# Performance work log

Hardware: AMD Instinct MI355X
Metric: run time of the kernel (lower is better)

The kernel has to match this reference:

```python
import jax, jax.numpy as jnp
import numpy as np

N_NODES = 50000
N_EDGES = 800000
IN_CH = 128
OUT_CH = 64
HEADS = 4
NEG_SLOPE = 0.2


def setup_inputs() -> dict:
    key = jax.random.key(0)
    k1, k2, k3, k4, k5, k6 = jax.random.split(key, 6)
    x = jax.random.normal(k1, (N_NODES, IN_CH), dtype=jnp.float32)
    edge_index = jax.random.randint(k2, (2, N_EDGES), 0, N_NODES, dtype=jnp.int64)
    # GATConv params (glorot-ish scale)
    W = jax.random.normal(k3, (HEADS * OUT_CH, IN_CH), dtype=jnp.float32) * (1.0 / np.sqrt(IN_CH))
    att_src = jax.random.normal(k4, (HEADS, OUT_CH), dtype=jnp.float32) * 0.1
    att_dst = jax.random.normal(k5, (HEADS, OUT_CH), dtype=jnp.float32) * 0.1
    bias = jax.random.normal(k6, (HEADS * OUT_CH,), dtype=jnp.float32) * 0.01
    return {"x": x, "edge_index": edge_index, "W": W, "att_src": att_src, "att_dst": att_dst, "bias": bias}


def reference(x, edge_index, W, att_src, att_dst, bias):
    N = x.shape[0]
    H, C = att_src.shape
    # add self loops (PyG GATConv default add_self_loops=True)
    loops = jnp.arange(N, dtype=edge_index.dtype)
    src = jnp.concatenate([edge_index[0], loops])  # [E+N]
    dst = jnp.concatenate([edge_index[1], loops])
    # linear projection -> [N, H, C]
    xl = (x @ W.T).reshape(N, H, C)
    # per-node attention logits [N, H]
    a_src = jnp.einsum('nhc,hc->nh', xl, att_src)
    a_dst = jnp.einsum('nhc,hc->nh', xl, att_dst)
    # edge-wise score, leaky relu
    alpha = jax.nn.leaky_relu(a_src[src] + a_dst[dst], NEG_SLOPE)  # [E+N, H]
    # segment softmax over destination nodes (every node has a self loop -> no empty segments)
    amax = jax.ops.segment_max(alpha, dst, num_segments=N)
    e = jnp.exp(alpha - amax[dst])
    denom = jax.ops.segment_sum(e, dst, num_segments=N)
    coef = e / denom[dst]  # [E+N, H]
    # weighted scatter-aggregate of source features
    out = jax.ops.segment_sum(coef[:, :, None] * xl[src], dst, num_segments=N)  # [N, H, C]
    out = out.reshape(N, H * C) + bias
    # last_layer=False -> ELU activation
    return jax.nn.elu(out)
```

## Files before the change

### kernel.cpp

```cpp
#include <hip/hip_runtime.h>
#include <hip/hip_bf16.h>
#include <math.h>

#define IN_C 128
#define HC   256
#define CH   64
#define NEG  0.2f

typedef __attribute__((ext_vector_type(8))) short short8;
typedef __attribute__((ext_vector_type(4))) float f32x4;
typedef __attribute__((ext_vector_type(2))) float f32x2;

#define TSTRIDE 264

__device__ __forceinline__ float lrelu(float v) { return v > 0.f ? v : NEG * v; }

__device__ __forceinline__ unsigned short f2bf(float f) {
    __hip_bfloat16 h = __float2bfloat16(f);
    return *reinterpret_cast<unsigned short*>(&h);
}
__device__ __forceinline__ unsigned pack2(float lo, float hi) {
    return (unsigned)f2bf(lo) | ((unsigned)f2bf(hi) << 16);
}

__device__ __forceinline__ void fma8pk(f32x2* acc, float wf, const uint4 u) {
    const f32x2 w2 = {wf, wf};
    f32x2 b;
    b.x = __uint_as_float(u.x << 16); b.y = __uint_as_float(u.x & 0xFFFF0000u);
    acc[0] = __builtin_elementwise_fma(w2, b, acc[0]);
    b.x = __uint_as_float(u.y << 16); b.y = __uint_as_float(u.y & 0xFFFF0000u);
    acc[1] = __builtin_elementwise_fma(w2, b, acc[1]);
    b.x = __uint_as_float(u.z << 16); b.y = __uint_as_float(u.z & 0xFFFF0000u);
    acc[2] = __builtin_elementwise_fma(w2, b, acc[2]);
    b.x = __uint_as_float(u.w << 16); b.y = __uint_as_float(u.w & 0xFFFF0000u);
    acc[3] = __builtin_elementwise_fma(w2, b, acc[3]);
}

__global__ void __launch_bounds__(256) k_gemm_deg(
    const float* __restrict__ x, const float* __restrict__ W,
    const float* __restrict__ att_src, const float* __restrict__ att_dst,
    const int* __restrict__ ei, int* __restrict__ deg, int* __restrict__ perm,
    __hip_bfloat16* __restrict__ xlb, float* __restrict__ asrc,
    float* __restrict__ adst, int N, int E, int DB)
{
    __shared__ short Wlds[256 * 128];

    const int t = threadIdx.x;

    if ((int)blockIdx.x < DB) {
        const int stride = DB * 256;
        for (int e = blockIdx.x * 256 + t; e < E; e += stride) {
            const int d = ei[E + e];
            perm[e] = atomicAdd(&deg[d], 1);
        }
        return;
    }

    const int bx   = blockIdx.x - DB;
    const int wv   = t >> 6;
    const int lane = t & 63;
    const int m    = lane & 15;
    const int quad = lane >> 4;
    const int r0   = bx * 64 + wv * 16;

#pragma unroll
    for (int i = 0; i < 16; ++i) {
        const int g   = t + 256 * i;
        const int row = g >> 4;
        const int c   = g & 15;
        const float4 wa = *(const float4*)&W[g * 8];
        const float4 wb = *(const float4*)&W[g * 8 + 4];
        uint4 v;
        v.x = pack2(wa.x, wa.y); v.y = pack2(wa.z, wa.w);
        v.z = pack2(wb.x, wb.y); v.w = pack2(wb.z, wb.w);
        *(uint4*)&Wlds[row * 128 + ((c ^ (row & 15)) * 8)] = v;
    }
    __syncthreads();

    f32x4 acc[16];
#pragma unroll
    for (int tc = 0; tc < 16; ++tc) acc[tc] = (f32x4){0.f, 0.f, 0.f, 0.f};

    const int arow = min(r0 + m, N - 1);
    const float* xrow = &x[(size_t)arow * IN_C];

#pragma unroll
    for (int kc = 0; kc < IN_C; kc += 32) {
        union { short8 v; unsigned u[4]; } a;
        const float4 xa = *(const float4*)&xrow[kc + quad * 8];
        const float4 xb = *(const float4*)&xrow[kc + quad * 8 + 4];
        a.u[0] = pack2(xa.x, xa.y); a.u[1] = pack2(xa.z, xa.w);
        a.u[2] = pack2(xb.x, xb.y); a.u[3] = pack2(xb.z, xb.w);
        const int kchunk = (kc >> 3) + quad;
        const int slotoff = ((kchunk ^ m) * 8);
#pragma unroll
        for (int tc = 0; tc < 16; ++tc) {
            const short8 b = *(const short8*)&Wlds[(tc * 16 + m) * 128 + slotoff];
            acc[tc] = __builtin_amdgcn_mfma_f32_16x16x32_bf16(a.v, b, acc[tc], 0, 0, 0);
        }
    }

    float as_l[16], ad_l[16];
#pragma unroll
    for (int tc = 0; tc < 16; ++tc) {
        as_l[tc] = att_src[tc * 16 + m];
        ad_l[tc] = att_dst[tc * 16 + m];
    }
#pragma unroll
    for (int i = 0; i < 4; ++i) {
        const int grow = r0 + quad * 4 + i;
        const bool ok = grow < N;
        float ps[4] = {0.f, 0.f, 0.f, 0.f};
        float pd[4] = {0.f, 0.f, 0.f, 0.f};
#pragma unroll
        for (int tc = 0; tc < 16; ++tc) {
            const float v = acc[tc][i];
            ps[tc >> 2] = fmaf(v, as_l[tc], ps[tc >> 2]);
            pd[tc >> 2] = fmaf(v, ad_l[tc], pd[tc >> 2]);
        }
#pragma unroll
        for (int msk = 1; msk < 16; msk <<= 1) {
#pragma unroll
            for (int hd = 0; hd < 4; ++hd) {
                ps[hd] += __shfl_xor(ps[hd], msk);
                pd[hd] += __shfl_xor(pd[hd], msk);
            }
        }
        if (m == 0 && ok) {
#pragma unroll
            for (int hd = 0; hd < 4; ++hd) {
                asrc[grow * 4 + hd] = ps[hd];
                adst[grow * 4 + hd] = pd[hd];
            }
        }
    }

    __syncthreads();
#pragma unroll
    for (int i = 0; i < 4; ++i) {
        const int lrow = wv * 16 + quad * 4 + i;
#pragma unroll
        for (int tc = 0; tc < 16; ++tc)
            Wlds[lrow * TSTRIDE + tc * 16 + m] = (short)f2bf(acc[tc][i]);
    }
    __syncthreads();
    const int r0blk = bx * 64;
#pragma unroll
    for (int k2 = 0; k2 < 8; ++k2) {
        const int c   = t + 256 * k2;
        const int row = c >> 5;
        const int off = c & 31;
        if (r0blk + row < N) {
            const uint4 v = *(const uint4*)&Wlds[row * TSTRIDE + off * 8];
            *(uint4*)&xlb[(size_t)(r0blk + row) * HC + off * 8] = v;
        }
    }
}

#define SCAN_TILE 2048
__global__ void __launch_bounds__(256) k_scan(
    const int* __restrict__ deg, int* __restrict__ offs,
    unsigned long long* __restrict__ tstat, int N, int E, int ntiles)
{
    __shared__ int sh[256];
    __shared__ int sh_base;
    const int tile = blockIdx.x;
    const int t = threadIdx.x;
    const int base = tile * SCAN_TILE + t * 8;

    int v[8];
    int tsum = 0;
#pragma unroll
    for (int j = 0; j < 8; ++j) {
        const int idx = base + j;
        v[j] = (idx < N) ? deg[idx] : 0;
        tsum += v[j];
    }
    sh[t] = tsum;
    __syncthreads();
    for (int off = 1; off < 256; off <<= 1) {
        const int u = (t >= off) ? sh[t - off] : 0;
        __syncthreads();
        sh[t] += u;
        __syncthreads();
    }
    const int blockSum = sh[255];
    const int texcl = sh[t] - tsum;

    if (t == 0) {
        int excl = 0;
        if (tile == 0) {
            __hip_atomic_store(&tstat[0], (2ull << 32) | (unsigned)blockSum,
                               __ATOMIC_RELEASE, __HIP_MEMORY_SCOPE_AGENT);
        } else {
            __hip_atomic_store(&tstat[tile], (1ull << 32) | (unsigned)blockSum,
                               __ATOMIC_RELEASE, __HIP_MEMORY_SCOPE_AGENT);
            int pb = tile - 1;
            while (true) {
                const unsigned long long st = __hip_atomic_load(&tstat[pb],
                        __ATOMIC_ACQUIRE, __HIP_MEMORY_SCOPE_AGENT);
                const unsigned state = (unsigned)(st >> 32);
                if (state == 0u) continue;
                excl += (int)(unsigned)(st & 0xFFFFFFFFu);
                if (state == 2u) break;
                --pb;
            }
            __hip_atomic_store(&tstat[tile],
                               (2ull << 32) | (unsigned)(excl + blockSum),
                               __ATOMIC_RELEASE, __HIP_MEMORY_SCOPE_AGENT);
        }
        sh_base = excl;
    }
    __syncthreads();
    int running = sh_base + texcl;
#pragma unroll
    for (int j = 0; j < 8; ++j) {
        const int idx = base + j;
        if (idx < N) offs[idx] = running;
        running += v[j];
    }
    if (tile == ntiles - 1 && t == 255) offs[N] = E;
}

__global__ void k_place(const int* __restrict__ ei, const int* __restrict__ perm,
                        const int* __restrict__ offs, int* __restrict__ csr_src, int E)
{
    int e = blockIdx.x * 256 + threadIdx.x;
    if (e >= E) return;
    int s = ei[e];
    int d = ei[E + e];
    csr_src[offs[d] + perm[e]] = s;
}

__global__ void __launch_bounds__(256, 8) k_agg(
    const __hip_bfloat16* __restrict__ xlb, const float* __restrict__ asrc,
    const float* __restrict__ adst, const int* __restrict__ offs,
    const int* __restrict__ csr_src, const float* __restrict__ bias,
    float* __restrict__ out, int N)
{
    const int t    = threadIdx.x;
    const int wv   = t >> 6;
    const int lane = t & 63;
    const int half = lane >> 5;
    const int li   = lane & 31;
    const int h    = li >> 3;
    const int n    = blockIdx.x * 4 + wv;
    if (n >= N) return;

    const float adn = adst[n * 4 + h];
    const int   p0 = offs[n];
    const int   pe = offs[n + 1];

    f32x2 acc[4];
#pragma unroll
    for (int q = 0; q < 4; ++q) acc[q] = (f32x2){0.f, 0.f};
    float l = 0.f;

    if (half == 0) {
        const float w = __expf(lrelu(asrc[n * 4 + h] + adn));
        const uint4 u = *(const uint4*)&xlb[(unsigned)n * HC + li * 8];
        fma8pk(acc, w, u);
        l = w;
    }

    int p = p0 + half;

    for (; p + 16 <= pe + half; p += 16) {
        int s[8];
#pragma unroll
        for (int j = 0; j < 8; ++j) s[j] = csr_src[p + 2 * j];
        uint4 u[8];
#pragma unroll
        for (int j = 0; j < 8; ++j)
            u[j] = *(const uint4*)&xlb[(unsigned)s[j] * HC + li * 8];
        float w[4];
#pragma unroll
        for (int j = 0; j < 4; ++j)
            w[j] = __expf(lrelu(asrc[s[j] * 4 + h] + adn));
#pragma unroll
        for (int j = 0; j < 4; ++j) { l += w[j]; fma8pk(acc, w[j], u[j]); }
#pragma unroll
        for (int j = 0; j < 4; ++j)
            w[j] = __expf(lrelu(asrc[s[j + 4] * 4 + h] + adn));
#pragma unroll
        for (int j = 0; j < 4; ++j) { l += w[j]; fma8pk(acc, w[j], u[j + 4]); }
    }
    for (; p + 8 <= pe + half; p += 8) {
        int s[4];
#pragma unroll
        for (int j = 0; j < 4; ++j) s[j] = csr_src[p + 2 * j];
        uint4 u[4];
#pragma unroll
        for (int j = 0; j < 4; ++j)
            u[j] = *(const uint4*)&xlb[(unsigned)s[j] * HC + li * 8];
#pragma unroll
        for (int j = 0; j < 4; ++j) {
            const float w = __expf(lrelu(asrc[s[j] * 4 + h] + adn));
            l += w;
            fma8pk(acc, w, u[j]);
        }
    }
    for (; p < pe; p += 2) {
        const int s0 = csr_src[p];
        const uint4 u0 = *(const uint4*)&xlb[(unsigned)s0 * HC + li * 8];
        const float w0 = __expf(lrelu(asrc[s0 * 4 + h] + adn));
        l += w0;
        fma8pk(acc, w0, u0);
    }

    l += __shfl_xor(l, 32);
#pragma unroll
    for (int q = 0; q < 4; ++q) {
        acc[q].x += __shfl_xor(acc[q].x, 32);
        acc[q].y += __shfl_xor(acc[q].y, 32);
    }
    const float inv = 1.0f / l;

    const int cbase = li * 8 + half * 4;
    const float4 bv = *(const float4*)&bias[cbase];
    f32x4 o;
    o.x = acc[half * 2 + 0].x * inv + bv.x;
    o.y = acc[half * 2 + 0].y * inv + bv.y;
    o.z = acc[half * 2 + 1].x * inv + bv.z;
    o.w = acc[half * 2 + 1].y * inv + bv.w;
    o.x = o.x > 0.f ? o.x : expm1f(o.x);
    o.y = o.y > 0.f ? o.y : expm1f(o.y);
    o.z = o.z > 0.f ? o.z : expm1f(o.z);
    o.w = o.w > 0.f ? o.w : expm1f(o.w);
    __builtin_nontemporal_store(o, (f32x4*)&out[(size_t)n * HC + cbase]);
}

extern "C" void kernel_launch(void* const* d_in, const int* in_sizes, int n_in,
                              void* d_out, int out_size, void* d_ws, size_t ws_size,
                              hipStream_t stream) {
    const float* x       = (const float*)d_in[0];
    const int*   ei      = (const int*)d_in[1];
    const float* W       = (const float*)d_in[2];
    const float* att_src = (const float*)d_in[3];
    const float* att_dst = (const float*)d_in[4];
    const float* bias    = (const float*)d_in[5];
    float* out = (float*)d_out;

    const int N = in_sizes[0] / IN_C;
    const int E = in_sizes[1] / 2;

    char* p = (char*)d_ws;
    auto alloc = [&](size_t bytes) -> char* {
        char* q = p;
        p += (bytes + 255) & ~(size_t)255;
        return q;
    };
    __hip_bfloat16* xlb = (__hip_bfloat16*)alloc((size_t)N * HC * 2);
    float* asrc = (float*)alloc((size_t)N * 4 * 4);
    float* adst = (float*)alloc((size_t)N * 4 * 4);
    int*   deg  = (int*)alloc((size_t)N * 4);
    unsigned long long* tstat = (unsigned long long*)alloc(4096);
    int*   offs = (int*)alloc((size_t)(N + 1) * 4);
    int*   perm = (int*)alloc((size_t)E * 4);
    int*   csr  = (int*)alloc((size_t)E * 4);

    const size_t degpad = ((size_t)N * 4 + 255) & ~(size_t)255;
    (void)hipMemsetAsync(deg, 0, degpad + 4096, stream);

    const int GB = (N + 63) / 64;
    const int DB = (E + 2047) / 2048;
    k_gemm_deg<<<DB + GB, 256, 0, stream>>>(x, W, att_src, att_dst,
                                            ei, deg, perm, xlb, asrc, adst, N, E, DB);

    const int ntiles = (N + SCAN_TILE - 1) / SCAN_TILE;
    k_scan<<<ntiles, 256, 0, stream>>>(deg, offs, tstat, N, E, ntiles);

    k_place<<<(E + 255) / 256, 256, 0, stream>>>(ei, perm, offs, csr, E);

    k_agg<<<(N + 3) / 4, 256, 0, stream>>>(xlb, asrc, adst, offs, csr, bias, out, N);
}
```

Before: 226.0 us.

## Pre-convert W to bf16 once and read B fragments from global in GEMM

Splits the fused GEMM+degree kernel into a degree-counting kernel, which also converts W to bf16 once, and a separate GEMM kernel. The GEMM now loads B fragments straight from the cached bf16 W in global memory instead of having every block stage and convert the 64KB W into LDS. That shrinks LDS to the transpose tile and raises occupancy (launch bounds 256,4). It adds a kernel launch and L2 traffic for B loads. k_place also becomes a grid-stride loop over 1024 blocks.

Result: slower. 261.3 us (+15.6%).

```diff
diff --git a/kernel.cpp b/kernel.cpp
--- a/kernel.cpp
+++ b/kernel.cpp
@@ -36,46 +36,44 @@
     acc[3] = __builtin_elementwise_fma(w2, b, acc[3]);
 }
 
-__global__ void __launch_bounds__(256) k_gemm_deg(
-    const float* __restrict__ x, const float* __restrict__ W,
+__global__ void __launch_bounds__(256) k_deg(
+    const float* __restrict__ W, short* __restrict__ Wb,
+    const int* __restrict__ ei, int* __restrict__ deg, int* __restrict__ perm,
+    int E, int WB)
+{
+    const int t = threadIdx.x;
+    if ((int)blockIdx.x < WB) {
+        const int i = (blockIdx.x * 256 + t) * 4;
+        const float4 v = *(const float4*)&W[i];
+        uint2 pk;
+        pk.x = pack2(v.x, v.y);
+        pk.y = pack2(v.z, v.w);
+        *(uint2*)&Wb[i] = pk;
+        return;
+    }
+    const int nb = gridDim.x - WB;
+    const int stride = nb * 256;
+    for (int e = (blockIdx.x - WB) * 256 + t; e < E; e += stride) {
+        const int d = ei[E + e];
+        perm[e] = atomicAdd(&deg[d], 1);
+    }
+}
+
+__global__ void __launch_bounds__(256, 4) k_gemm(
+    const float* __restrict__ x, const short* __restrict__ Wb,
     const float* __restrict__ att_src, const float* __restrict__ att_dst,
-    const int* __restrict__ ei, int* __restrict__ deg, int* __restrict__ perm,
     __hip_bfloat16* __restrict__ xlb, float* __restrict__ asrc,
-    float* __restrict__ adst, int N, int E, int DB)
-{
-    __shared__ short Wlds[256 * 128];
-
-    const int t = threadIdx.x;
-
-    if ((int)blockIdx.x < DB) {
-        const int stride = DB * 256;
-        for (int e = blockIdx.x * 256 + t; e < E; e += stride) {
-            const int d = ei[E + e];
-            perm[e] = atomicAdd(&deg[d], 1);
-        }
-        return;
-    }
-
-    const int bx   = blockIdx.x - DB;
+    float* __restrict__ adst, int N)
+{
+    __shared__ short Tlds[64 * TSTRIDE];
+
+    const int t    = threadIdx.x;
+    const int bx   = blockIdx.x;
     const int wv   = t >> 6;
     const int lane = t & 63;
     const int m    = lane & 15;
     const int quad = lane >> 4;
     const int r0   = bx * 64 + wv * 16;
-
-#pragma unroll
-    for (int i = 0; i < 16; ++i) {
-        const int g   = t + 256 * i;
-        const int row = g >> 4;
-        const int c   = g & 15;
-        const float4 wa = *(const float4*)&W[g * 8];
-        const float4 wb = *(const float4*)&W[g * 8 + 4];
-        uint4 v;
-        v.x = pack2(wa.x, wa.y); v.y = pack2(wa.z, wa.w);
-        v.z = pack2(wb.x, wb.y); v.w = pack2(wb.z, wb.w);
-        *(uint4*)&Wlds[row * 128 + ((c ^ (row & 15)) * 8)] = v;
-    }
-    __syncthreads();
 
     f32x4 acc[16];
 #pragma unroll
@@ -91,12 +89,17 @@
         const float4 xb = *(const float4*)&xrow[kc + quad * 8 + 4];
         a.u[0] = pack2(xa.x, xa.y); a.u[1] = pack2(xa.z, xa.w);
         a.u[2] = pack2(xb.x, xb.y); a.u[3] = pack2(xb.z, xb.w);
-        const int kchunk = (kc >> 3) + quad;
-        const int slotoff = ((kchunk ^ m) * 8);
-#pragma unroll
-        for (int tc = 0; tc < 16; ++tc) {
-            const short8 b = *(const short8*)&Wlds[(tc * 16 + m) * 128 + slotoff];
-            acc[tc] = __builtin_amdgcn_mfma_f32_16x16x32_bf16(a.v, b, acc[tc], 0, 0, 0);
+        const short* bbase = &Wb[(size_t)m * IN_C + (((kc >> 3) + quad) * 8)];
+#pragma unroll
+        for (int th = 0; th < 2; ++th) {
+            short8 b[8];
+#pragma unroll
+            for (int j = 0; j < 8; ++j)
+                b[j] = *(const short8*)&bbase[(size_t)(th * 8 + j) * 16 * IN_C];
+#pragma unroll
+            for (int j = 0; j < 8; ++j)
+                acc[th * 8 + j] = __builtin_amdgcn_mfma_f32_16x16x32_bf16(
+                    a.v, b[j], acc[th * 8 + j], 0, 0, 0);
         }
     }
 
@@ -135,13 +138,12 @@
         }
     }
 
-    __syncthreads();
 #pragma unroll
     for (int i = 0; i < 4; ++i) {
         const int lrow = wv * 16 + quad * 4 + i;
 #pragma unroll
         for (int tc = 0; tc < 16; ++tc)
-            Wlds[lrow * TSTRIDE + tc * 16 + m] = (short)f2bf(acc[tc][i]);
+            Tlds[lrow * TSTRIDE + tc * 16 + m] = (short)f2bf(acc[tc][i]);
     }
     __syncthreads();
     const int r0blk = bx * 64;
@@ -151,7 +153,7 @@
         const int row = c >> 5;
         const int off = c & 31;
         if (r0blk + row < N) {
-            const uint4 v = *(const uint4*)&Wlds[row * TSTRIDE + off * 8];
+            const uint4 v = *(const uint4*)&Tlds[row * TSTRIDE + off * 8];
             *(uint4*)&xlb[(size_t)(r0blk + row) * HC + off * 8] = v;
         }
     }
@@ -222,14 +224,16 @@
     if (tile == ntiles - 1 && t == 255) offs[N] = E;
 }
 
-__global__ void k_place(const int* __restrict__ ei, const int* __restrict__ perm,
-                        const int* __restrict__ offs, int* __restrict__ csr_src, int E)
-{
-    int e = blockIdx.x * 256 + threadIdx.x;
-    if (e >= E) return;
-    int s = ei[e];
-    int d = ei[E + e];
-    csr_src[offs[d] + perm[e]] = s;
+__global__ void __launch_bounds__(256) k_place(
+    const int* __restrict__ ei, const int* __restrict__ perm,
+    const int* __restrict__ offs, int* __restrict__ csr_src, int E)
+{
+    const int stride = gridDim.x * 256;
+    for (int e = blockIdx.x * 256 + threadIdx.x; e < E; e += stride) {
+        const int s = ei[e];
+        const int d = ei[E + e];
+        csr_src[offs[d] + perm[e]] = s;
+    }
 }
 
 __global__ void __launch_bounds__(256, 8) k_agg(
@@ -343,6 +347,7 @@
 
     const int N = in_sizes[0] / IN_C;
     const int E = in_sizes[1] / 2;
+    const int W_ELEMS = HC * IN_C;
 
     char* p = (char*)d_ws;
     auto alloc = [&](size_t bytes) -> char* {
@@ -351,6 +356,7 @@
         return q;
     };
     __hip_bfloat16* xlb = (__hip_bfloat16*)alloc((size_t)N * HC * 2);
+    short* Wb   = (short*)alloc((size_t)W_ELEMS * 2);
     float* asrc = (float*)alloc((size_t)N * 4 * 4);
     float* adst = (float*)alloc((size_t)N * 4 * 4);
     int*   deg  = (int*)alloc((size_t)N * 4);
@@ -362,15 +368,16 @@
     const size_t degpad = ((size_t)N * 4 + 255) & ~(size_t)255;
     (void)hipMemsetAsync(deg, 0, degpad + 4096, stream);
 
+    const int WB = W_ELEMS / (256 * 4);
+    k_deg<<<WB + 1024, 256, 0, stream>>>(W, Wb, ei, deg, perm, E, WB);
+
     const int GB = (N + 63) / 64;
-    const int DB = (E + 2047) / 2048;
-    k_gemm_deg<<<DB + GB, 256, 0, stream>>>(x, W, att_src, att_dst,
-                                            ei, deg, perm, xlb, asrc, adst, N, E, DB);
+    k_gemm<<<GB, 256, 0, stream>>>(x, Wb, att_src, att_dst, xlb, asrc, adst, N);
 
     const int ntiles = (N + SCAN_TILE - 1) / SCAN_TILE;
     k_scan<<<ntiles, 256, 0, stream>>>(deg, offs, tstat, N, E, ntiles);
 
-    k_place<<<(E + 255) / 256, 256, 0, stream>>>(ei, perm, offs, csr, E);
+    k_place<<<1024, 256, 0, stream>>>(ei, perm, offs, csr, E);
 
     k_agg<<<(N + 3) / 4, 256, 0, stream>>>(xlb, asrc, adst, offs, csr, bias, out, N);
 }
```
